# Kernel optimization log

Hardware: AMD Instinct MI355X
Metric: run time of the kernel (lower is better)

The kernel has to match this reference:

```python
import jax, jax.numpy as jnp
import numpy as np

KW = 3          # kernel_width
PAD = (KW - 1) // 2


def setup_inputs() -> dict:
    key = jax.random.key(0)
    ks = jax.random.split(key, 7)
    B, QL, KL, QS, KS = 16, 1024, 1024, 512, 512
    q = jax.random.normal(ks[0], (B, QL, QS), dtype=jnp.float32)
    k = jax.random.normal(ks[1], (B, KL, KS), dtype=jnp.float32)
    # torch Linear weights: [out_features, in_features]
    Wk = jax.random.normal(ks[2], (KS * KW, QS), dtype=jnp.float32) * (1.0 / np.sqrt(QS))
    bk = jax.random.normal(ks[3], (KS * KW,), dtype=jnp.float32) * 0.02
    Wb = jax.random.normal(ks[4], (1, QS), dtype=jnp.float32) * (1.0 / np.sqrt(QS))
    bb = jax.random.normal(ks[5], (1,), dtype=jnp.float32) * 0.02
    bias_b = jax.random.normal(ks[6], (1,), dtype=jnp.float32)
    return {"q": q, "k": k, "Wk": Wk, "bk": bk, "Wb": Wb, "bb": bb, "bias_b": bias_b}


def reference(q, k, Wk, bk, Wb, bb, bias_b):
    B, QL, QS = q.shape
    _, KL, KS = k.shape
    # per-query dynamic kernels: [B, QL, KS, KW]
    kernel = (jnp.einsum('biq,oq->bio', q, Wk) + bk).reshape(B, QL, KS, KW)
    # per-query scalar bias: [B, QL]
    bias = (jnp.einsum('biq,oq->bio', q, Wb) + bb)[..., 0]
    # banded multiply-accumulate, equivalent to grouped conv1d with groups=B
    k_pad = jnp.pad(k, ((0, 0), (PAD, PAD), (0, 0)))  # [B, KL+KW-1, KS]
    # windows[b, j, t, c] = k_pad[b, j+t, c]  -> [B, KL, KW, KS]
    windows = jnp.stack([k_pad[:, t:t + KL, :] for t in range(KW)], axis=2)
    scores = jnp.einsum('bict,bjtc->bij', kernel, windows)
    return scores + bias[:, :, None] + bias_b[0]
```

## Files before the change

kernel.cpp:

```cpp
#include <hip/hip_runtime.h>

typedef unsigned short ushort_t;
typedef unsigned int uint32;
typedef __bf16 bf16x8 __attribute__((ext_vector_type(8)));
typedef float f32x4 __attribute__((ext_vector_type(4)));
typedef float f4 __attribute__((ext_vector_type(4)));
typedef unsigned short us4 __attribute__((ext_vector_type(4)));


__device__ __forceinline__ ushort_t f2bf(float f) {
    uint32 u = __builtin_bit_cast(uint32, f);
    u = (u + 0x7fffu + ((u >> 16) & 1u)) >> 16;
    return (ushort_t)u;
}

#define FULL_BAR() do { __builtin_amdgcn_sched_barrier(0); __builtin_amdgcn_s_barrier(); __builtin_amdgcn_sched_barrier(0); } while (0)
#define HALF_BAR() do { __builtin_amdgcn_sched_barrier(0); __builtin_amdgcn_s_barrier(); } while (0)

__global__ __launch_bounds__(256) void prep_all(const float* __restrict__ q,
                                                const float* __restrict__ Wb,
                                                const float* __restrict__ bb,
                                                const float* __restrict__ k,
                                                const float* __restrict__ Wk,
                                                const float* __restrict__ bk,
                                                ushort_t* __restrict__ qb,
                                                float* __restrict__ biasw,
                                                ushort_t* __restrict__ kbp,
                                                ushort_t* __restrict__ wkb,
                                                float* __restrict__ bkp) {
    const int tid = threadIdx.x;
    if (blockIdx.x < 4096) {
        const int lane = tid & 63, wid = tid >> 6;
        const int m = blockIdx.x * 4 + wid;
        const float* qrow = q + (size_t)m * 512;

        f4 v0 = *(const f4*)(qrow + lane * 4);
        f4 v1 = *(const f4*)(qrow + 256 + lane * 4);
        f4 w0 = *(const f4*)(Wb + lane * 4);
        f4 w1 = *(const f4*)(Wb + 256 + lane * 4);

        float dot = v0[0]*w0[0] + v0[1]*w0[1] + v0[2]*w0[2] + v0[3]*w0[3]
                  + v1[0]*w1[0] + v1[1]*w1[1] + v1[2]*w1[2] + v1[3]*w1[3];

        us4 o0, o1;
        o0[0]=f2bf(v0[0]); o0[1]=f2bf(v0[1]); o0[2]=f2bf(v0[2]); o0[3]=f2bf(v0[3]);
        o1[0]=f2bf(v1[0]); o1[1]=f2bf(v1[1]); o1[2]=f2bf(v1[2]); o1[3]=f2bf(v1[3]);
        *(us4*)(qb + (size_t)m * 512 + lane * 4) = o0;
        *(us4*)(qb + (size_t)m * 512 + 256 + lane * 4) = o1;

        #pragma unroll
        for (int off = 32; off >= 1; off >>= 1) dot += __shfl_xor(dot, off);
        if (lane == 0) biasw[m] = dot + bb[0];
        return;
    }
    const int gid = (blockIdx.x - 4096) * 256 + tid;
    if (gid < 1536) bkp[gid] = bk[(gid & 511) * 3 + (gid >> 9)];

    const int KG = (16 * 1024 * 512) / 4;
    const int PG = (16 * 2 * 512) / 4;

    if (gid < KG) {
        const int e = gid * 4;
        const int b = e >> 19;
        const int rem = e & ((1 << 19) - 1);
        const int row = rem >> 9, c = rem & 511;
        f4 v = *(const f4*)(k + e);
        us4 o; o[0]=f2bf(v[0]); o[1]=f2bf(v[1]); o[2]=f2bf(v[2]); o[3]=f2bf(v[3]);
        *(us4*)(kbp + ((size_t)b * 1026 + row + 1) * 512 + c) = o;
    } else if (gid < KG + PG) {
        const int p = gid - KG;
        const int b = p >> 8, off = p & 255;
        const int row = (off < 128) ? 0 : 1025;
        const int c = (off & 127) * 4;
        us4 z; z[0]=0; z[1]=0; z[2]=0; z[3]=0;
        *(us4*)(kbp + ((size_t)b * 1026 + row) * 512 + c) = z;
    } else {
        const int w = gid - KG - PG;
        const int n = w >> 7;
        const int c = (w & 127) * 4;
        const int o = (n & 511) * 3 + (n >> 9);
        f4 v = *(const f4*)(Wk + (size_t)o * 512 + c);
        us4 ov; ov[0]=f2bf(v[0]); ov[1]=f2bf(v[1]); ov[2]=f2bf(v[2]); ov[3]=f2bf(v[3]);
        *(us4*)(wkb + (size_t)n * 512 + c) = ov;
    }
}


__device__ __forceinline__ void stage16k(const char* base, int ld, char* dst, int tid) {
    #pragma unroll
    for (int inst = 0; inst < 2; ++inst) {
        const int idx = inst * 512 + tid;
        const int srow = idx >> 2;
        const int scol = ((idx & 3) ^ ((idx >> 3) & 3)) << 4;
        __builtin_amdgcn_global_load_lds(
            (const __attribute__((address_space(1))) void*)(base + (size_t)srow * (size_t)ld + scol),
            (__attribute__((address_space(3))) void*)(dst + (inst * 512 + (tid & ~63)) * 16),
            16, 0, 0);
    }
}

#define GEMM_CORE(NT, A_OFF, B_OFF, A_LD, B_LD)                                            \
    stage16k(Ag + (size_t)(A_OFF(0)), A_LD, lds, tid);                                     \
    stage16k(Bg + (size_t)(B_OFF(0)), B_LD, lds + 16384, tid);                             \
    stage16k(Ag + (size_t)(A_OFF(1)), A_LD, lds + 32768, tid);                             \
    stage16k(Bg + (size_t)(B_OFF(1)), B_LD, lds + 32768 + 16384, tid);                     \
    stage16k(Ag + (size_t)(A_OFF(2)), A_LD, lds + 65536, tid);                             \
    stage16k(Bg + (size_t)(B_OFF(2)), B_LD, lds + 65536 + 16384, tid);                     \
    asm volatile("s_waitcnt vmcnt(8)" ::: "memory");                                       \
    FULL_BAR();                                                                            \
    for (int t = 0; t < NT; ++t) {                                                         \
        const char* lA = lds + ((t & 3) << 15);                                            \
        const char* lB = lA + 16384;                                                       \
        char* nb = lds + (((t + 3) & 3) << 15);                                            \
        const int tn3 = (t + 3 < NT) ? t + 3 : NT - 1;                                     \
        bf16x8 a[4], a2[4], b[4];                                                          \
        _Pragma("unroll")                                                                  \
        for (int mi = 0; mi < 4; ++mi) a[mi] = *(const bf16x8*)(lA + wrA + mi * 1024);     \
        _Pragma("unroll")                                                                  \
        for (int ni = 0; ni < 4; ++ni) b[ni] = *(const bf16x8*)(lB + wcB + ni * 1024);     \
        stage16k(Ag + (size_t)(A_OFF(tn3)), A_LD, nb, tid);                                \
        FULL_BAR();                                                                        \
        __builtin_amdgcn_s_setprio(1);                                                     \
        _Pragma("unroll")                                                                  \
        for (int mi = 0; mi < 4; ++mi)                                                     \
            _Pragma("unroll")                                                              \
            for (int ni = 0; ni < 4; ++ni)                                                 \
                acc[mi][ni] = __builtin_amdgcn_mfma_f32_16x16x32_bf16(a[mi], b[ni], acc[mi][ni], 0, 0, 0); \
        __builtin_amdgcn_s_setprio(0);                                                     \
        HALF_BAR();                                                                        \
        _Pragma("unroll")                                                                  \
        for (int mi = 0; mi < 4; ++mi) a2[mi] = *(const bf16x8*)(lA + wrA + (4 + mi) * 1024); \
        stage16k(Bg + (size_t)(B_OFF(tn3)), B_LD, nb + 16384, tid);                        \
        asm volatile("s_waitcnt vmcnt(8)" ::: "memory");                                   \
        FULL_BAR();                                                                        \
        __builtin_amdgcn_s_setprio(1);                                                     \
        _Pragma("unroll")                                                                  \
        for (int mi = 0; mi < 4; ++mi)                                                     \
            _Pragma("unroll")                                                              \
            for (int ni = 0; ni < 4; ++ni)                                                 \
                acc[4 + mi][ni] = __builtin_amdgcn_mfma_f32_16x16x32_bf16(a2[mi], b[ni], acc[4 + mi][ni], 0, 0, 0); \
        __builtin_amdgcn_s_setprio(0);                                                     \
        HALF_BAR();                                                                        \
    }

#define A1OFF(tt) ((tt) * 64)
#define B1OFF(tt) ((tt) * 64)
#define A2OFF(tt) ((tt) * 64)
#define B2OFF(tt) (((tt) >> 4) * 1024 + ((tt) & 15) * 64)

__global__ __launch_bounds__(512) void gemm1(const ushort_t* __restrict__ qb,
                                             const ushort_t* __restrict__ wkb,
                                             const float* __restrict__ bkp,
                                             ushort_t* __restrict__ coef) {
    __shared__ alignas(16) char lds[131072];
    const int tid = threadIdx.x;
    const int l = tid & 63, wid = tid >> 6;
    const int wr = wid >> 2, wc = wid & 3;
    int bid = blockIdx.x;
    bid = (bid & 7) * 48 + (bid >> 3);
    const int mt = bid & 63, nt = bid >> 6;
    const int mbase = mt * 256, nbase = nt * 256;

    const char* Ag = (const char*)(qb + (size_t)mbase * 512);
    const char* Bg = (const char*)(wkb + (size_t)nbase * 512);

    const int r15 = l & 15, q = l >> 4;
    const int laneoff = r15 * 64 + (((q ^ (r15 >> 1)) & 3) << 4);
    const int wrA = wr * 8192 + laneoff;
    const int wcB = wc * 4096 + laneoff;

    f32x4 acc[8][4];
    #pragma unroll
    for (int mi = 0; mi < 8; ++mi)
        #pragma unroll
        for (int ni = 0; ni < 4; ++ni)
            #pragma unroll
            for (int r = 0; r < 4; ++r) acc[mi][ni][r] = 0.f;

    GEMM_CORE(16, A1OFF, B1OFF, 1024, 1024)

    #pragma unroll
    for (int ni = 0; ni < 4; ++ni) {
        const int ncol = nbase + wc * 64 + ni * 16 + r15;
        const float bkv = bkp[ncol];
        #pragma unroll
        for (int mi = 0; mi < 8; ++mi) {
            const int mrow0 = mbase + wr * 128 + mi * 16 + q * 4;
            #pragma unroll
            for (int r = 0; r < 4; ++r)
                coef[(size_t)(mrow0 + r) * 1536 + ncol] = f2bf(acc[mi][ni][r] + bkv);
        }
    }
}

__global__ __launch_bounds__(512) void gemm2(const ushort_t* __restrict__ coef,
                                             const ushort_t* __restrict__ kbp,
                                             const float* __restrict__ biasw,
                                             const float* __restrict__ bias_b,
                                             float* __restrict__ out) {
    __shared__ alignas(16) char lds[131072];
    const int tid = threadIdx.x;
    const int l = tid & 63, wid = tid >> 6;
    const int wr = wid >> 2, wc = wid & 3;
    int bid = blockIdx.x;
    bid = (bid & 7) * 32 + (bid >> 3);
    const int jt = bid & 3, it = (bid >> 2) & 3, b = bid >> 4;
    const int ibase = it * 256, jbase = jt * 256;

    const char* Ag = (const char*)(coef + ((size_t)b * 1024 + ibase) * 1536);
    const char* Bg = (const char*)(kbp + ((size_t)b * 1026 + jbase) * 512);

    const int r15 = l & 15, q = l >> 4;
    const int laneoff = r15 * 64 + (((q ^ (r15 >> 1)) & 3) << 4);
    const int wrA = wr * 8192 + laneoff;
    const int wcB = wc * 4096 + laneoff;

    f32x4 acc[8][4];
    #pragma unroll
    for (int mi = 0; mi < 8; ++mi)
        #pragma unroll
        for (int ni = 0; ni < 4; ++ni)
            #pragma unroll
            for (int r = 0; r < 4; ++r) acc[mi][ni][r] = 0.f;

    GEMM_CORE(48, A2OFF, B2OFF, 3072, 1024)

    const float bb0v = bias_b[0];
    #pragma unroll
    for (int mi = 0; mi < 8; ++mi) {
        const int irow0 = ibase + wr * 128 + mi * 16 + q * 4;
        #pragma unroll
        for (int r = 0; r < 4; ++r) {
            const float bv = biasw[b * 1024 + irow0 + r] + bb0v;
            #pragma unroll
            for (int ni = 0; ni < 4; ++ni) {
                const int jcol = jbase + wc * 64 + ni * 16 + r15;
                out[((size_t)b << 20) + (size_t)(irow0 + r) * 1024 + jcol] = acc[mi][ni][r] + bv;
            }
        }
    }
}

extern "C" void kernel_launch(void* const* d_in, const int* in_sizes, int n_in,
                              void* d_out, int out_size, void* d_ws, size_t ws_size,
                              hipStream_t stream) {
    const float* q      = (const float*)d_in[0];
    const float* k      = (const float*)d_in[1];
    const float* Wk     = (const float*)d_in[2];
    const float* bk     = (const float*)d_in[3];
    const float* Wb     = (const float*)d_in[4];
    const float* bb     = (const float*)d_in[5];
    const float* bias_b = (const float*)d_in[6];
    float* out = (float*)d_out;

    ushort_t* ws   = (ushort_t*)d_ws;
    ushort_t* qb   = ws;
    ushort_t* kbp  = qb  + (size_t)16384 * 512;
    ushort_t* wkb  = kbp + (size_t)16 * 1026 * 512;
    ushort_t* coef = wkb + (size_t)1536 * 512;
    float*    biasw = (float*)(coef + (size_t)16384 * 1536);
    float*    bkp   = biasw + 16384;

    prep_all<<<13072, 256, 0, stream>>>(q, Wb, bb, k, Wk, bk, qb, biasw, kbp, wkb, bkp);
    gemm1<<<384, 512, 0, stream>>>(qb, wkb, bkp, coef);
    gemm2<<<256, 512, 0, stream>>>(coef, kbp, biasw, bias_b, out);
}
```

Before: 226.7 us.

## Restructure GEMM pipelines to double-buffered 64-wide K halves and smaller gemm1 tiles

Replaces the shared 4-stage 32-K pipeline macro with explicit double-buffered pipelines that stage 64-wide K steps in two halves and interleave loads with MFMA clusters. gemm1 moves from 256x256 to 128x256 tiles with 768 blocks and smaller LDS, so more blocks are in flight and the tail is better balanced. gemm2 keeps 256x256 tiles but uses fewer, larger iterations with an adjusted swizzle. This trades pipeline depth (two buffers instead of four) for fewer barriers per K element, plus an explicit lgkmcnt wait before each MFMA cluster.

After: 216.7 us. -4.4%, faster.

```diff
diff --git a/kernel.cpp b/kernel.cpp
--- a/kernel.cpp
+++ b/kernel.cpp
@@ -16,6 +16,11 @@
 
 #define FULL_BAR() do { __builtin_amdgcn_sched_barrier(0); __builtin_amdgcn_s_barrier(); __builtin_amdgcn_sched_barrier(0); } while (0)
 #define HALF_BAR() do { __builtin_amdgcn_sched_barrier(0); __builtin_amdgcn_s_barrier(); } while (0)
+#define PRE_MFMA() do { __builtin_amdgcn_sched_barrier(0); __builtin_amdgcn_s_barrier(); \
+    asm volatile("s_waitcnt lgkmcnt(0)" ::: "memory"); __builtin_amdgcn_sched_barrier(0); } while (0)
+
+#define AS1 __attribute__((address_space(1)))
+#define AS3 __attribute__((address_space(3)))
 
 __global__ __launch_bounds__(256) void prep_all(const float* __restrict__ q,
                                                 const float* __restrict__ Wb,
@@ -85,107 +90,104 @@
     }
 }
 
-
-__device__ __forceinline__ void stage16k(const char* base, int ld, char* dst, int tid) {
-    #pragma unroll
-    for (int inst = 0; inst < 2; ++inst) {
+template<int NINST>
+__device__ __forceinline__ void stage_half(const char* base, int ld, char* dst, int tid) {
+    #pragma unroll
+    for (int inst = 0; inst < NINST; ++inst) {
         const int idx = inst * 512 + tid;
-        const int srow = idx >> 2;
-        const int scol = ((idx & 3) ^ ((idx >> 3) & 3)) << 4;
+        const int row = idx >> 2;
+        const int scol = ((idx & 3) ^ ((row >> 1) & 3)) << 4;
         __builtin_amdgcn_global_load_lds(
-            (const __attribute__((address_space(1))) void*)(base + (size_t)srow * (size_t)ld + scol),
-            (__attribute__((address_space(3))) void*)(dst + (inst * 512 + (tid & ~63)) * 16),
+            (const AS1 void*)(base + (size_t)row * (size_t)ld + scol),
+            (AS3 void*)(dst + (size_t)(inst * 512 + (tid & ~63)) * 16),
             16, 0, 0);
     }
 }
 
-#define GEMM_CORE(NT, A_OFF, B_OFF, A_LD, B_LD)                                            \
-    stage16k(Ag + (size_t)(A_OFF(0)), A_LD, lds, tid);                                     \
-    stage16k(Bg + (size_t)(B_OFF(0)), B_LD, lds + 16384, tid);                             \
-    stage16k(Ag + (size_t)(A_OFF(1)), A_LD, lds + 32768, tid);                             \
-    stage16k(Bg + (size_t)(B_OFF(1)), B_LD, lds + 32768 + 16384, tid);                     \
-    stage16k(Ag + (size_t)(A_OFF(2)), A_LD, lds + 65536, tid);                             \
-    stage16k(Bg + (size_t)(B_OFF(2)), B_LD, lds + 65536 + 16384, tid);                     \
-    asm volatile("s_waitcnt vmcnt(8)" ::: "memory");                                       \
-    FULL_BAR();                                                                            \
-    for (int t = 0; t < NT; ++t) {                                                         \
-        const char* lA = lds + ((t & 3) << 15);                                            \
-        const char* lB = lA + 16384;                                                       \
-        char* nb = lds + (((t + 3) & 3) << 15);                                            \
-        const int tn3 = (t + 3 < NT) ? t + 3 : NT - 1;                                     \
-        bf16x8 a[4], a2[4], b[4];                                                          \
-        _Pragma("unroll")                                                                  \
-        for (int mi = 0; mi < 4; ++mi) a[mi] = *(const bf16x8*)(lA + wrA + mi * 1024);     \
-        _Pragma("unroll")                                                                  \
-        for (int ni = 0; ni < 4; ++ni) b[ni] = *(const bf16x8*)(lB + wcB + ni * 1024);     \
-        stage16k(Ag + (size_t)(A_OFF(tn3)), A_LD, nb, tid);                                \
-        FULL_BAR();                                                                        \
-        __builtin_amdgcn_s_setprio(1);                                                     \
-        _Pragma("unroll")                                                                  \
-        for (int mi = 0; mi < 4; ++mi)                                                     \
-            _Pragma("unroll")                                                              \
-            for (int ni = 0; ni < 4; ++ni)                                                 \
-                acc[mi][ni] = __builtin_amdgcn_mfma_f32_16x16x32_bf16(a[mi], b[ni], acc[mi][ni], 0, 0, 0); \
-        __builtin_amdgcn_s_setprio(0);                                                     \
-        HALF_BAR();                                                                        \
-        _Pragma("unroll")                                                                  \
-        for (int mi = 0; mi < 4; ++mi) a2[mi] = *(const bf16x8*)(lA + wrA + (4 + mi) * 1024); \
-        stage16k(Bg + (size_t)(B_OFF(tn3)), B_LD, nb + 16384, tid);                        \
-        asm volatile("s_waitcnt vmcnt(8)" ::: "memory");                                   \
-        FULL_BAR();                                                                        \
-        __builtin_amdgcn_s_setprio(1);                                                     \
-        _Pragma("unroll")                                                                  \
-        for (int mi = 0; mi < 4; ++mi)                                                     \
-            _Pragma("unroll")                                                              \
-            for (int ni = 0; ni < 4; ++ni)                                                 \
-                acc[4 + mi][ni] = __builtin_amdgcn_mfma_f32_16x16x32_bf16(a2[mi], b[ni], acc[4 + mi][ni], 0, 0, 0); \
-        __builtin_amdgcn_s_setprio(0);                                                     \
-        HALF_BAR();                                                                        \
-    }
-
-#define A1OFF(tt) ((tt) * 64)
-#define B1OFF(tt) ((tt) * 64)
-#define A2OFF(tt) ((tt) * 64)
-#define B2OFF(tt) (((tt) >> 4) * 1024 + ((tt) & 15) * 64)
+#define MFMA_CLUSTER(af, bf, accrow)                                         \
+    __builtin_amdgcn_s_setprio(1);                                           \
+    _Pragma("unroll")                                                        \
+    for (int i_ = 0; i_ < 4; ++i_)                                           \
+        _Pragma("unroll")                                                    \
+        for (int j_ = 0; j_ < 4; ++j_)                                       \
+            acc[(accrow) + i_][j_] = __builtin_amdgcn_mfma_f32_16x16x32_bf16( \
+                af[i_], bf[j_], acc[(accrow) + i_][j_], 0, 0, 0);            \
+    __builtin_amdgcn_s_setprio(0);
 
 __global__ __launch_bounds__(512) void gemm1(const ushort_t* __restrict__ qb,
                                              const ushort_t* __restrict__ wkb,
                                              const float* __restrict__ bkp,
                                              ushort_t* __restrict__ coef) {
-    __shared__ alignas(16) char lds[131072];
+    __shared__ alignas(16) char lds[98304];
     const int tid = threadIdx.x;
     const int l = tid & 63, wid = tid >> 6;
     const int wr = wid >> 2, wc = wid & 3;
     int bid = blockIdx.x;
-    bid = (bid & 7) * 48 + (bid >> 3);
-    const int mt = bid & 63, nt = bid >> 6;
-    const int mbase = mt * 256, nbase = nt * 256;
+    bid = (bid & 7) * 96 + (bid >> 3);
+    const int mt = bid & 127, nt = bid >> 7;
+    const int mbase = mt * 128, nbase = nt * 256;
 
     const char* Ag = (const char*)(qb + (size_t)mbase * 512);
     const char* Bg = (const char*)(wkb + (size_t)nbase * 512);
 
     const int r15 = l & 15, q = l >> 4;
-    const int laneoff = r15 * 64 + (((q ^ (r15 >> 1)) & 3) << 4);
-    const int wrA = wr * 8192 + laneoff;
-    const int wcB = wc * 4096 + laneoff;
-
-    f32x4 acc[8][4];
-    #pragma unroll
-    for (int mi = 0; mi < 8; ++mi)
+    const int swz = ((q ^ (r15 >> 1)) & 3) << 4;
+    const int laneA = (wr * 64 + r15) * 64 + swz;
+    const int laneB = (wc * 64 + r15) * 64 + swz;
+
+    f32x4 acc[4][4];
+    #pragma unroll
+    for (int mi = 0; mi < 4; ++mi)
         #pragma unroll
         for (int ni = 0; ni < 4; ++ni)
             #pragma unroll
             for (int r = 0; r < 4; ++r) acc[mi][ni][r] = 0.f;
 
-    GEMM_CORE(16, A1OFF, B1OFF, 1024, 1024)
+    stage_half<1>(Ag, 1024, lds, tid);
+    stage_half<2>(Bg, 1024, lds + 16384, tid);
+    stage_half<1>(Ag + 64, 1024, lds + 8192, tid);
+    stage_half<2>(Bg + 64, 1024, lds + 32768, tid);
+    asm volatile("s_waitcnt vmcnt(3)" ::: "memory");
+    FULL_BAR();
+
+    for (int t = 0; t < 8; ++t) {
+        const char* bA = lds + ((t & 1) ? 49152 : 0);
+        char* nb = lds + ((t & 1) ? 0 : 49152);
+        const int tn = (t < 7) ? t + 1 : t;
+        const size_t off = (size_t)tn * 128;
+
+        bf16x8 a0[4], b0[4];
+        #pragma unroll
+        for (int i = 0; i < 4; ++i) a0[i] = *(const bf16x8*)(bA + laneA + i * 1024);
+        #pragma unroll
+        for (int j = 0; j < 4; ++j) b0[j] = *(const bf16x8*)(bA + 16384 + laneB + j * 1024);
+        stage_half<1>(Ag + off, 1024, nb, tid);
+        stage_half<2>(Bg + off, 1024, nb + 16384, tid);
+        asm volatile("s_waitcnt vmcnt(3)" ::: "memory");
+        PRE_MFMA();
+        MFMA_CLUSTER(a0, b0, 0)
+        HALF_BAR();
+
+        bf16x8 a1[4], b1[4];
+        #pragma unroll
+        for (int i = 0; i < 4; ++i) a1[i] = *(const bf16x8*)(bA + 8192 + laneA + i * 1024);
+        #pragma unroll
+        for (int j = 0; j < 4; ++j) b1[j] = *(const bf16x8*)(bA + 32768 + laneB + j * 1024);
+        stage_half<1>(Ag + off + 64, 1024, nb + 8192, tid);
+        stage_half<2>(Bg + off + 64, 1024, nb + 32768, tid);
+        asm volatile("s_waitcnt vmcnt(3)" ::: "memory");
+        PRE_MFMA();
+        MFMA_CLUSTER(a1, b1, 0)
+        HALF_BAR();
+    }
 
     #pragma unroll
     for (int ni = 0; ni < 4; ++ni) {
         const int ncol = nbase + wc * 64 + ni * 16 + r15;
         const float bkv = bkp[ncol];
         #pragma unroll
-        for (int mi = 0; mi < 8; ++mi) {
-            const int mrow0 = mbase + wr * 128 + mi * 16 + q * 4;
+        for (int mi = 0; mi < 4; ++mi) {
+            const int mrow0 = mbase + wr * 64 + mi * 16 + q * 4;
             #pragma unroll
             for (int r = 0; r < 4; ++r)
                 coef[(size_t)(mrow0 + r) * 1536 + ncol] = f2bf(acc[mi][ni][r] + bkv);
@@ -211,9 +213,9 @@
     const char* Bg = (const char*)(kbp + ((size_t)b * 1026 + jbase) * 512);
 
     const int r15 = l & 15, q = l >> 4;
-    const int laneoff = r15 * 64 + (((q ^ (r15 >> 1)) & 3) << 4);
-    const int wrA = wr * 8192 + laneoff;
-    const int wcB = wc * 4096 + laneoff;
+    const int swz = ((q ^ (r15 >> 1)) & 3) << 4;
+    const int laneA = (wr * 128 + r15) * 64 + swz;
+    const int laneB = (wc * 64 + r15) * 64 + swz;
 
     f32x4 acc[8][4];
     #pragma unroll
@@ -223,7 +225,58 @@
             #pragma unroll
             for (int r = 0; r < 4; ++r) acc[mi][ni][r] = 0.f;
 
-    GEMM_CORE(48, A2OFF, B2OFF, 3072, 1024)
+    stage_half<2>(Ag, 3072, lds, tid);
+    stage_half<2>(Bg, 1024, lds + 32768, tid);
+    stage_half<2>(Ag + 64, 3072, lds + 16384, tid);
+    stage_half<2>(Bg + 64, 1024, lds + 49152, tid);
+    asm volatile("s_waitcnt vmcnt(4)" ::: "memory");
+    FULL_BAR();
+
+    for (int t = 0; t < 24; ++t) {
+        const char* bA = lds + ((t & 1) << 16);
+        char* nb = lds + (((t + 1) & 1) << 16);
+        const int tn = (t < 23) ? t + 1 : t;
+        const size_t aoff = (size_t)tn * 128;
+        const size_t boff = (size_t)(tn >> 3) * 1024 + (size_t)(tn & 7) * 128;
+
+        bf16x8 a0[4], b0[4];
+        #pragma unroll
+        for (int i = 0; i < 4; ++i) a0[i] = *(const bf16x8*)(bA + laneA + i * 1024);
+        #pragma unroll
+        for (int j = 0; j < 4; ++j) b0[j] = *(const bf16x8*)(bA + 32768 + laneB + j * 1024);
+        stage_half<2>(Ag + aoff, 3072, nb, tid);
+        PRE_MFMA();
+        MFMA_CLUSTER(a0, b0, 0)
+        HALF_BAR();
+
+        bf16x8 a1[4];
+        #pragma unroll
+        for (int i = 0; i < 4; ++i) a1[i] = *(const bf16x8*)(bA + laneA + (4 + i) * 1024);
+        stage_half<2>(Bg + boff, 1024, nb + 32768, tid);
+        asm volatile("s_waitcnt vmcnt(4)" ::: "memory");
+        PRE_MFMA();
+        MFMA_CLUSTER(a1, b0, 4)
+        HALF_BAR();
+
+        bf16x8 a2[4], b1[4];
+        #pragma unroll
+        for (int i = 0; i < 4; ++i) a2[i] = *(const bf16x8*)(bA + 16384 + laneA + i * 1024);
+        #pragma unroll
+        for (int j = 0; j < 4; ++j) b1[j] = *(const bf16x8*)(bA + 49152 + laneB + j * 1024);
+        stage_half<2>(Ag + aoff + 64, 3072, nb + 16384, tid);
+        PRE_MFMA();
+        MFMA_CLUSTER(a2, b1, 0)
+        HALF_BAR();
+
+        bf16x8 a3[4];
+        #pragma unroll
+        for (int i = 0; i < 4; ++i) a3[i] = *(const bf16x8*)(bA + 16384 + laneA + (4 + i) * 1024);
+        stage_half<2>(Bg + boff + 64, 1024, nb + 49152, tid);
+        asm volatile("s_waitcnt vmcnt(4)" ::: "memory");
+        PRE_MFMA();
+        MFMA_CLUSTER(a3, b1, 4)
+        HALF_BAR();
+    }
 
     const float bb0v = bias_b[0];
     #pragma unroll
@@ -262,6 +315,6 @@
     float*    bkp   = biasw + 16384;
 
     prep_all<<<13072, 256, 0, stream>>>(q, Wb, bb, k, Wk, bk, qb, biasw, kbp, wkb, bkp);
-    gemm1<<<384, 512, 0, stream>>>(qb, wkb, bkp, coef);
+    gemm1<<<768, 512, 0, stream>>>(qb, wkb, bkp, coef);
     gemm2<<<256, 512, 0, stream>>>(coef, kbp, biasw, bias_b, out);
 }
```
